# Kernel optimization log

Hardware: AMD Instinct MI355X
Metric: run time of the kernel (lower is better)

The kernel has to match this reference:

```python
import jax, jax.numpy as jnp
import numpy as np

HIDDEN = 2048
FFN = 8192
NUM_EXPERTS = 8
TOP_K = 2


def setup_inputs() -> dict:
    key = jax.random.key(0)
    ks = jax.random.split(key, 6)
    scale_h = 1.0 / np.sqrt(HIDDEN)
    scale_f = 1.0 / np.sqrt(FFN)
    return {
        "hidden_states": jax.random.normal(ks[0], (4, 2048, HIDDEN), jnp.float32),
        "gate_w": jax.random.normal(ks[1], (NUM_EXPERTS, HIDDEN), jnp.float32) * scale_h,
        "w1": jax.random.normal(ks[2], (NUM_EXPERTS, HIDDEN, FFN), jnp.float32) * scale_h,
        "b1": jax.random.normal(ks[3], (NUM_EXPERTS, FFN), jnp.float32) * 0.01,
        "w2": jax.random.normal(ks[4], (NUM_EXPERTS, FFN, HIDDEN), jnp.float32) * scale_f,
        "b2": jax.random.normal(ks[5], (NUM_EXPERTS, HIDDEN), jnp.float32) * 0.01,
    }


def reference(hidden_states, gate_w, w1, b1, w2, b2):
    B, S, H = hidden_states.shape
    E = gate_w.shape[0]
    tokens = hidden_states.reshape(-1, H)  # [T, H]

    # Router: softmax gate, top-2, renormalize selected weights
    logits = tokens @ gate_w.T  # [T, E]
    probs = jax.nn.softmax(logits, axis=-1)
    topk_w, topk_idx = jax.lax.top_k(probs, TOP_K)  # [T, 2]
    topk_w = topk_w / jnp.sum(topk_w, axis=-1, keepdims=True)

    # Dense combine weights: w_dense[t, e] = routing weight of token t for expert e
    w_dense = jnp.sum(jax.nn.one_hot(topk_idx, E, dtype=topk_w.dtype) * topk_w[..., None], axis=1)  # [T, E]

    # Per-expert FFN (exact GELU as nn.GELU default), weighted scatter-combine
    combined = jnp.zeros_like(tokens)
    for e in range(E):  # small fixed expert count
        h = jax.nn.gelu(tokens @ w1[e] + b1[e], approximate=False)  # [T, F]
        combined = combined + w_dense[:, e:e + 1] * (h @ w2[e] + b2[e])

    return combined.reshape(B, S, H) + hidden_states
```

## Files before the change

### kernel.cpp

```cpp
#include <hip/hip_runtime.h>
#include <hip/hip_bf16.h>

#define T_TOK 8192
#define HID 2048
#define FFN_ 8192
#define NE 8
#define MAXR 18432

typedef __attribute__((ext_vector_type(8))) short bf16x8;
typedef __attribute__((ext_vector_type(4))) float f32x4;
typedef __attribute__((ext_vector_type(8))) unsigned short u16x8;

__device__ __forceinline__ unsigned short f2bf(float f) {
  unsigned int u = __float_as_uint(f);
  u += 0x7fffu + ((u >> 16) & 1u);
  return (unsigned short)(u >> 16);
}
__device__ __forceinline__ float bf2f(unsigned short h) {
  return __uint_as_float(((unsigned int)h) << 16);
}

__device__ __forceinline__ void gload_lds16(const ushort* g, ushort* l) {
  __builtin_amdgcn_global_load_lds(
      (const __attribute__((address_space(1))) unsigned int*)g,
      (__attribute__((address_space(3))) unsigned int*)l, 16, 0, 0);
}

__global__ __launch_bounds__(256) void router_kernel(
    const float* __restrict__ x, const float* __restrict__ gw,
    int* __restrict__ topk_idx, float* __restrict__ topk_w, int* __restrict__ counts)
{
  int lane = threadIdx.x & 63;
  int w = threadIdx.x >> 6;
  int t = blockIdx.x * 4 + w;
  const float* xr = x + (size_t)t * HID;
  float acc[NE];
#pragma unroll
  for (int e = 0; e < NE; ++e) acc[e] = 0.f;
  for (int h = lane; h < HID; h += 64) {
    float xv = xr[h];
#pragma unroll
    for (int e = 0; e < NE; ++e) acc[e] = fmaf(xv, gw[e * HID + h], acc[e]);
  }
#pragma unroll
  for (int e = 0; e < NE; ++e) {
#pragma unroll
    for (int s = 32; s > 0; s >>= 1) acc[e] += __shfl_xor(acc[e], s);
  }
  if (lane == 0) {
    int i0 = 0; float v0 = acc[0];
#pragma unroll
    for (int e = 1; e < NE; ++e) { if (acc[e] > v0) { v0 = acc[e]; i0 = e; } }
    int i1 = -1; float v1 = -3.4e38f;
#pragma unroll
    for (int e = 0; e < NE; ++e) { if (e != i0 && acc[e] > v1) { v1 = acc[e]; i1 = e; } }
    float r = __expf(v1 - v0);
    float w0 = 1.f / (1.f + r);
    float w1 = r * w0;
    topk_idx[2 * t] = i0; topk_idx[2 * t + 1] = i1;
    topk_w[2 * t] = w0;   topk_w[2 * t + 1] = w1;
    atomicAdd(&counts[i0], 1);
    atomicAdd(&counts[i1], 1);
  }
}

__global__ void offsets_kernel(const int* __restrict__ counts, int* __restrict__ offs) {
  if (threadIdx.x == 0 && blockIdx.x == 0) {
    int o = 0;
#pragma unroll
    for (int e = 0; e < NE; ++e) { offs[e] = o; o += (counts[e] + 255) & ~255; }
    offs[NE] = o;
  }
}

__global__ __launch_bounds__(256) void scatter_kernel(
    const int* __restrict__ topk_idx, const float* __restrict__ topk_w,
    const int* __restrict__ offs, int* __restrict__ cursors,
    int* __restrict__ slot_token, float* __restrict__ slot_w, int* __restrict__ token_slot)
{
  int t = blockIdx.x * blockDim.x + threadIdx.x;
  if (t >= T_TOK) return;
#pragma unroll
  for (int k = 0; k < 2; ++k) {
    int e = topk_idx[2 * t + k];
    int pos = atomicAdd(&cursors[e], 1);
    int slot = offs[e] + pos;
    slot_token[slot] = t;
    slot_w[slot] = topk_w[2 * t + k];
    token_slot[2 * t + k] = slot;
  }
}

__global__ __launch_bounds__(256) void gather_kernel(
    const float* __restrict__ x, const int* __restrict__ slot_token, ushort* __restrict__ Xg)
{
  int row = blockIdx.x;
  int tok = slot_token[row];
  ushort* dst = Xg + (size_t)row * HID + threadIdx.x * 8;
  if (tok < 0) {
    u16x8 z = {0, 0, 0, 0, 0, 0, 0, 0};
    *(u16x8*)dst = z;
  } else {
    const float* s = x + (size_t)tok * HID + threadIdx.x * 8;
    float4 a = *(const float4*)s;
    float4 b = *(const float4*)(s + 4);
    u16x8 v;
    v[0] = f2bf(a.x); v[1] = f2bf(a.y); v[2] = f2bf(a.z); v[3] = f2bf(a.w);
    v[4] = f2bf(b.x); v[5] = f2bf(b.y); v[6] = f2bf(b.z); v[7] = f2bf(b.w);
    *(u16x8*)dst = v;
  }
}

__global__ __launch_bounds__(256) void transpose_convert_kernel(
    const float* __restrict__ src, ushort* __restrict__ dst, int R, int C)
{
  __shared__ float tile[64][65];
  int e = blockIdx.z;
  const float* s = src + (size_t)e * R * C;
  ushort* d = dst + (size_t)e * R * C;
  int r0 = blockIdx.y << 6, c0 = blockIdx.x << 6;
  int t = threadIdx.x;
#pragma unroll
  for (int i = 0; i < 4; ++i) {
    int idx = i * 256 + t;
    int row = idx >> 4;
    int c4 = (idx & 15) << 2;
    float4 v = *(const float4*)&s[(size_t)(r0 + row) * C + (c0 + c4)];
    tile[row][c4 + 0] = v.x; tile[row][c4 + 1] = v.y;
    tile[row][c4 + 2] = v.z; tile[row][c4 + 3] = v.w;
  }
  __syncthreads();
#pragma unroll
  for (int i = 0; i < 8; ++i) {
    int idx = (i * 256 + t) * 2;
    int orow = idx >> 6;
    int ocol = idx & 63;
    ushort2 p;
    p.x = f2bf(tile[ocol][orow]);
    p.y = f2bf(tile[ocol + 1][orow]);
    *(ushort2*)&d[(size_t)(c0 + orow) * R + (r0 + ocol)] = p;
  }
}


#define WAIT_LGKM() do { asm volatile("s_waitcnt lgkmcnt(0)" ::: "memory"); \
                         __builtin_amdgcn_sched_barrier(0); } while (0)
#define WAIT_VM6()  do { asm volatile("s_waitcnt vmcnt(6)" ::: "memory");  \
                         __builtin_amdgcn_sched_barrier(0); } while (0)
#define WAIT_VM0()  do { asm volatile("s_waitcnt vmcnt(0)" ::: "memory");  \
                         __builtin_amdgcn_sched_barrier(0); } while (0)

#define STG_A(BUF, HALF, T) do {                                            \
    ushort* _d = lds + (BUF) * 32768 + (HALF) * 8192 + tid * 8;             \
    gload_lds16(sA0 + (size_t)(HALF) * 64 * K + (size_t)(T) * 64, _d);      \
    gload_lds16(sA1 + (size_t)(HALF) * 64 * K + (size_t)(T) * 64, _d + 4096); \
  } while (0)
#define STG_B(BUF, HALF, T) do {                                            \
    ushort* _d = lds + (BUF) * 32768 + 16384 + (HALF) * 8192 + tid * 8;     \
    gload_lds16(sB0 + (size_t)(HALF) * 32 * K + (size_t)(T) * 64, _d);      \
    gload_lds16(sB1 + (size_t)(HALF) * 32 * K + (size_t)(T) * 64, _d + 4096); \
  } while (0)

#define LDA(BUF, MQ) do {                                                   \
    _Pragma("unroll") for (int mm = 0; mm < 4; ++mm) {                      \
      const ushort* _p = lds + (BUF) * 32768 + (MQ) * 8192 + aoff + mm * 1024; \
      af[mm][0] = *(const bf16x8*)(_p + ck0);                               \
      af[mm][1] = *(const bf16x8*)(_p + ck1);                               \
    } } while (0)
#define LDB(BUF, NQ) do {                                                   \
    _Pragma("unroll") for (int nn = 0; nn < 2; ++nn) {                      \
      const ushort* _p = lds + (BUF) * 32768 + 16384 + (NQ) * 8192 + boff + nn * 1024; \
      bf[NQ][nn][0] = *(const bf16x8*)(_p + ck0);                           \
      bf[NQ][nn][1] = *(const bf16x8*)(_p + ck1);                           \
    } } while (0)

#define MFMA_Q(MQ, NQ) do {                                                 \
    _Pragma("unroll") for (int mm = 0; mm < 4; ++mm)                        \
    _Pragma("unroll") for (int nn = 0; nn < 2; ++nn) {                      \
      acc[(MQ)*4+mm][(NQ)*2+nn] = __builtin_amdgcn_mfma_f32_16x16x32_bf16(  \
          af[mm][0], bf[NQ][nn][0], acc[(MQ)*4+mm][(NQ)*2+nn], 0, 0, 0);    \
      acc[(MQ)*4+mm][(NQ)*2+nn] = __builtin_amdgcn_mfma_f32_16x16x32_bf16(  \
          af[mm][1], bf[NQ][nn][1], acc[(MQ)*4+mm][(NQ)*2+nn], 0, 0, 0);    \
    } } while (0)

#define PH_MFMA(MQ, NQ) do {                                                \
    __builtin_amdgcn_s_barrier();                                           \
    WAIT_LGKM();                                                            \
    __builtin_amdgcn_s_setprio(1);                                          \
    MFMA_Q(MQ, NQ);                                                         \
    __builtin_amdgcn_s_setprio(0);                                          \
    __builtin_amdgcn_sched_barrier(0);                                      \
  } while (0)

template <int EPI>
__global__ __launch_bounds__(512, 2) void gemm256_kernel(
    const ushort* __restrict__ A, const ushort* __restrict__ Bt,
    const float* __restrict__ bias, ushort* __restrict__ Cout,
    const float* __restrict__ slot_w, const int* __restrict__ offs,
    int K, int N, int gx)
{
  __shared__ ushort lds[65536];

  const int tid = threadIdx.x;
  int nwg = gridDim.x * gridDim.y;
  int wg = blockIdx.y * gridDim.x + blockIdx.x;
  int cpx = nwg >> 3;
  wg = (wg & 7) * cpx + (wg >> 3);
  int rb = wg / gx, cb = wg - rb * gx;

  int total = offs[NE];
  int row0 = rb * 256;
  if (row0 >= total) return;
  int e = 0;
#pragma unroll
  for (int i = 1; i < NE; ++i) e += (row0 >= offs[i]) ? 1 : 0;

  const ushort* Ag = A + (size_t)row0 * K;
  const ushort* Bg = Bt + ((size_t)e * N + (size_t)cb * 256) * K;

  const int pr0 = tid >> 3;
  const int pr1 = 64 + pr0;
  const int j0 = (tid & 7) ^ (pr0 & 7);
  const int j1 = (tid & 7) ^ (pr1 & 7);
  const int rA0 = pr0;
  const int rA1 = 128 + pr0;
  const int rB0 = ((pr0 >> 5) << 6) + (pr0 & 31);
  const int rB1 = ((pr1 >> 5) << 6) + (pr1 & 31);
  const ushort* sA0 = Ag + (size_t)rA0 * K + j0 * 8;
  const ushort* sA1 = Ag + (size_t)rA1 * K + j1 * 8;
  const ushort* sB0 = Bg + (size_t)rB0 * K + j0 * 8;
  const ushort* sB1 = Bg + (size_t)rB1 * K + j1 * 8;

  const int lane = tid & 63;
  const int wid = tid >> 6;
  const int wr = wid >> 2, wc = wid & 3;
  const int lrow = lane & 15, g = lane >> 4, x7 = lrow & 7;
  const int ck0 = (g ^ x7) * 8;
  const int ck1 = ((4 + g) ^ x7) * 8;
  const int aoff = (wr * 64 + lrow) * 64;
  const int boff = (wc * 32 + lrow) * 64;

  f32x4 acc[8][4] = {};
  bf16x8 af[4][2], bf[2][2][2];

  const int NT = K >> 6;
  const int NITER = NT >> 1;

  STG_A(0, 0, 0); STG_A(0, 1, 0); STG_B(0, 0, 0); STG_B(0, 1, 0);
  STG_A(1, 0, 1); STG_B(1, 0, 1); STG_B(1, 1, 1);
  WAIT_VM6();
  __builtin_amdgcn_s_barrier();

  for (int it = 0; it < NITER; ++it) {
    const int tb = 2 * it + 1;
    const int tn0 = 2 * it + 2;
    const int tn1 = 2 * it + 3;
    const bool more0 = tn0 < NT;
    const bool more1 = tn1 < NT;

    LDA(0, 0); LDB(0, 0);
    STG_A(1, 1, tb);
    PH_MFMA(0, 0);
    __builtin_amdgcn_s_barrier();

    LDB(0, 1);
    if (more0) STG_A(0, 0, tn0);
    PH_MFMA(0, 1);
    __builtin_amdgcn_s_barrier();

    LDA(0, 1);
    if (more0) STG_B(0, 0, tn0);
    PH_MFMA(1, 0);
    __builtin_amdgcn_s_barrier();

    if (more0) STG_B(0, 1, tn0);
    PH_MFMA(1, 1);
    if (it + 1 < NITER) { WAIT_VM6(); } else { WAIT_VM0(); }
    __builtin_amdgcn_s_barrier();

    LDA(1, 0); LDB(1, 0);
    if (more0) STG_A(0, 1, tn0);
    PH_MFMA(0, 0);
    __builtin_amdgcn_s_barrier();

    LDB(1, 1);
    if (more1) STG_A(1, 0, tn1);
    PH_MFMA(0, 1);
    __builtin_amdgcn_s_barrier();

    LDA(1, 1);
    if (more1) STG_B(1, 0, tn1);
    PH_MFMA(1, 0);
    __builtin_amdgcn_s_barrier();

    if (more1) STG_B(1, 1, tn1);
    PH_MFMA(1, 1);
    if (more1) WAIT_VM6();
    __builtin_amdgcn_s_barrier();
  }

  const int colb = cb * 256 + wc * 64;
  const int rowb = row0 + wr * 128;
#pragma unroll
  for (int n = 0; n < 4; ++n) {
    const int nq = n >> 1, nn = n & 1;
    const int gc = colb + nq * 32 + nn * 16 + lrow;
    const float bv = bias[(size_t)e * N + gc];
#pragma unroll
    for (int m = 0; m < 8; ++m) {
      const int mq = m >> 2, mm = m & 3;
      const int gr = rowb + mq * 64 + mm * 16 + g * 4;
#pragma unroll
      for (int i = 0; i < 4; ++i) {
        float v = acc[m][n][i] + bv;
        if (EPI == 0) {
          v = 0.5f * v * (1.f + erff(v * 0.70710678118654752f));
        } else {
          v *= slot_w[gr + i];
        }
        Cout[(size_t)(gr + i) * N + gc] = f2bf(v);
      }
    }
  }
}

__global__ __launch_bounds__(256) void combine_kernel(
    const float* __restrict__ x, const ushort* __restrict__ Yp,
    const int* __restrict__ token_slot, float* __restrict__ out)
{
  int t = blockIdx.x;
  int s0 = token_slot[2 * t], s1 = token_slot[2 * t + 1];
  int c = threadIdx.x * 8;
  const float* xr = x + (size_t)t * HID + c;
  u16x8 y0 = *(const u16x8*)&Yp[(size_t)s0 * HID + c];
  u16x8 y1 = *(const u16x8*)&Yp[(size_t)s1 * HID + c];
  float4 xa = *(const float4*)xr;
  float4 xb = *(const float4*)(xr + 4);
  float4 oa, ob;
  oa.x = xa.x + bf2f(y0[0]) + bf2f(y1[0]);
  oa.y = xa.y + bf2f(y0[1]) + bf2f(y1[1]);
  oa.z = xa.z + bf2f(y0[2]) + bf2f(y1[2]);
  oa.w = xa.w + bf2f(y0[3]) + bf2f(y1[3]);
  ob.x = xb.x + bf2f(y0[4]) + bf2f(y1[4]);
  ob.y = xb.y + bf2f(y0[5]) + bf2f(y1[5]);
  ob.z = xb.z + bf2f(y0[6]) + bf2f(y1[6]);
  ob.w = xb.w + bf2f(y0[7]) + bf2f(y1[7]);
  float* orow = out + (size_t)t * HID + c;
  *(float4*)orow = oa;
  *(float4*)(orow + 4) = ob;
}

extern "C" void kernel_launch(void* const* d_in, const int* in_sizes, int n_in,
                              void* d_out, int out_size, void* d_ws, size_t ws_size,
                              hipStream_t stream)
{
  const float* x  = (const float*)d_in[0];
  const float* gw = (const float*)d_in[1];
  const float* w1 = (const float*)d_in[2];
  const float* b1 = (const float*)d_in[3];
  const float* w2 = (const float*)d_in[4];
  const float* b2 = (const float*)d_in[5];
  float* out = (float*)d_out;

  char* ws = (char*)d_ws;
  ushort* wT  = (ushort*)(ws + 0);
  ushort* Hb  = (ushort*)(ws + 268435456);
  ushort* Xg  = (ushort*)(ws + 570425344);
  ushort* Yp  = Xg;
  char* sm = ws + 645922816;
  int*   slot_token = (int*)(sm);
  float* slot_w     = (float*)(sm + 73728);
  int*   token_slot = (int*)(sm + 147456);
  int*   topk_idx   = (int*)(sm + 212992);
  float* topk_w     = (float*)(sm + 278528);
  int*   counts     = (int*)(sm + 344064);
  int*   cursors    = (int*)(sm + 344096);
  int*   offs       = (int*)(sm + 344128);

  hipMemsetAsync(counts, 0, 64, stream);
  hipMemsetAsync(slot_token, 0xFF, MAXR * 4, stream);

  router_kernel<<<dim3(T_TOK / 4), dim3(256), 0, stream>>>(x, gw, topk_idx, topk_w, counts);
  offsets_kernel<<<dim3(1), dim3(64), 0, stream>>>(counts, offs);
  scatter_kernel<<<dim3(T_TOK / 256), dim3(256), 0, stream>>>(
      topk_idx, topk_w, offs, cursors, slot_token, slot_w, token_slot);
  gather_kernel<<<dim3(MAXR), dim3(256), 0, stream>>>(x, slot_token, Xg);

  transpose_convert_kernel<<<dim3(FFN_ / 64, HID / 64, NE), dim3(256), 0, stream>>>(
      w1, wT, HID, FFN_);
  gemm256_kernel<0><<<dim3(FFN_ / 256, MAXR / 256), dim3(512), 0, stream>>>(
      Xg, wT, b1, Hb, nullptr, offs, HID, FFN_, FFN_ / 256);

  transpose_convert_kernel<<<dim3(HID / 64, FFN_ / 64, NE), dim3(256), 0, stream>>>(
      w2, wT, FFN_, HID);
  gemm256_kernel<1><<<dim3(HID / 256, MAXR / 256), dim3(512), 0, stream>>>(
      Hb, wT, b2, Yp, slot_w, offs, FFN_, HID, HID / 256);

  combine_kernel<<<dim3(T_TOK), dim3(256), 0, stream>>>(x, Yp, token_slot, out);
}
```

Measured before the change: 2.036 ms.

## Software-pipeline LDS fragment loads with double-buffered registers and remap tile raster

Restructures the GEMM main loop so the A/B fragments for the next MFMA phase are read from LDS into a second register set while the current phase computes, with one barrier per phase instead of two. The 2D grid becomes a 1D grid with an explicit XCD-aware mapping that keeps column blocks per XCD and iterates row blocks inside. The exact erf GELU is replaced with a tanh approximation built on a fast exp. The changes raise register pressure, make the barrier and wait ordering more delicate, and alter numerics slightly.

Result: slower. 2.713 ms (+33.2%).

```diff
diff --git a/kernel.cpp b/kernel.cpp
--- a/kernel.cpp
+++ b/kernel.cpp
@@ -24,6 +24,16 @@
   __builtin_amdgcn_global_load_lds(
       (const __attribute__((address_space(1))) unsigned int*)g,
       (__attribute__((address_space(3))) unsigned int*)l, 16, 0, 0);
+}
+
+__device__ __forceinline__ float gelu_f(float v) {
+  float u = v * (0.7978845608f + 0.0356774081f * v * v);
+  float a = fabsf(u);
+  float ex = __expf(-2.f * a);
+  float r = 1.f / (1.f + ex);
+  float th = (1.f - ex) * r;
+  th = (u >= 0.f) ? th : -th;
+  return 0.5f * v * (1.f + th);
 }
 
 __global__ __launch_bounds__(256) void router_kernel(
@@ -143,12 +153,10 @@
 }
 
 
-#define WAIT_LGKM() do { asm volatile("s_waitcnt lgkmcnt(0)" ::: "memory"); \
-                         __builtin_amdgcn_sched_barrier(0); } while (0)
-#define WAIT_VM6()  do { asm volatile("s_waitcnt vmcnt(6)" ::: "memory");  \
-                         __builtin_amdgcn_sched_barrier(0); } while (0)
-#define WAIT_VM0()  do { asm volatile("s_waitcnt vmcnt(0)" ::: "memory");  \
-                         __builtin_amdgcn_sched_barrier(0); } while (0)
+#define VMW6() asm volatile("s_waitcnt vmcnt(6)" ::: "memory")
+#define VMW0() asm volatile("s_waitcnt vmcnt(0)" ::: "memory")
+#define SCB()  __builtin_amdgcn_sched_barrier(0)
+#define BAR()  __builtin_amdgcn_s_barrier()
 
 #define STG_A(BUF, HALF, T) do {                                            \
     ushort* _d = lds + (BUF) * 32768 + (HALF) * 8192 + tid * 8;             \
@@ -161,35 +169,31 @@
     gload_lds16(sB1 + (size_t)(HALF) * 32 * K + (size_t)(T) * 64, _d + 4096); \
   } while (0)
 
-#define LDA(BUF, MQ) do {                                                   \
+#define LDA_INTO(SET, BUF, MQ) do {                                         \
     _Pragma("unroll") for (int mm = 0; mm < 4; ++mm) {                      \
       const ushort* _p = lds + (BUF) * 32768 + (MQ) * 8192 + aoff + mm * 1024; \
-      af[mm][0] = *(const bf16x8*)(_p + ck0);                               \
-      af[mm][1] = *(const bf16x8*)(_p + ck1);                               \
+      af##SET[mm][0] = *(const bf16x8*)(_p + ck0);                          \
+      af##SET[mm][1] = *(const bf16x8*)(_p + ck1);                          \
     } } while (0)
-#define LDB(BUF, NQ) do {                                                   \
+#define LDB_INTO(NQ, BUF) do {                                              \
     _Pragma("unroll") for (int nn = 0; nn < 2; ++nn) {                      \
       const ushort* _p = lds + (BUF) * 32768 + 16384 + (NQ) * 8192 + boff + nn * 1024; \
       bf[NQ][nn][0] = *(const bf16x8*)(_p + ck0);                           \
       bf[NQ][nn][1] = *(const bf16x8*)(_p + ck1);                           \
     } } while (0)
 
-#define MFMA_Q(MQ, NQ) do {                                                 \
+#define MFMAQ(SET, MQ, NQ) do {                                             \
+    SCB();                                                                  \
+    __builtin_amdgcn_s_setprio(1);                                          \
     _Pragma("unroll") for (int mm = 0; mm < 4; ++mm)                        \
     _Pragma("unroll") for (int nn = 0; nn < 2; ++nn) {                      \
       acc[(MQ)*4+mm][(NQ)*2+nn] = __builtin_amdgcn_mfma_f32_16x16x32_bf16(  \
-          af[mm][0], bf[NQ][nn][0], acc[(MQ)*4+mm][(NQ)*2+nn], 0, 0, 0);    \
+          af##SET[mm][0], bf[NQ][nn][0], acc[(MQ)*4+mm][(NQ)*2+nn], 0, 0, 0); \
       acc[(MQ)*4+mm][(NQ)*2+nn] = __builtin_amdgcn_mfma_f32_16x16x32_bf16(  \
-          af[mm][1], bf[NQ][nn][1], acc[(MQ)*4+mm][(NQ)*2+nn], 0, 0, 0);    \
-    } } while (0)
-
-#define PH_MFMA(MQ, NQ) do {                                                \
-    __builtin_amdgcn_s_barrier();                                           \
-    WAIT_LGKM();                                                            \
-    __builtin_amdgcn_s_setprio(1);                                          \
-    MFMA_Q(MQ, NQ);                                                         \
+          af##SET[mm][1], bf[NQ][nn][1], acc[(MQ)*4+mm][(NQ)*2+nn], 0, 0, 0); \
+    }                                                                       \
     __builtin_amdgcn_s_setprio(0);                                          \
-    __builtin_amdgcn_sched_barrier(0);                                      \
+    SCB(); BAR(); SCB();                                                    \
   } while (0)
 
 template <int EPI>
@@ -197,16 +201,16 @@
     const ushort* __restrict__ A, const ushort* __restrict__ Bt,
     const float* __restrict__ bias, ushort* __restrict__ Cout,
     const float* __restrict__ slot_w, const int* __restrict__ offs,
-    int K, int N, int gx)
+    int K, int N, int gx, int gy)
 {
   __shared__ ushort lds[65536];
 
   const int tid = threadIdx.x;
-  int nwg = gridDim.x * gridDim.y;
-  int wg = blockIdx.y * gridDim.x + blockIdx.x;
-  int cpx = nwg >> 3;
-  wg = (wg & 7) * cpx + (wg >> 3);
-  int rb = wg / gx, cb = wg - rb * gx;
+  int b = blockIdx.x;
+  int xcd = b & 7, s = b >> 3;
+  int sc = s / gy;
+  int cb = xcd * (gx >> 3) + sc;
+  int rb = s - sc * gy;
 
   int total = offs[NE];
   int row0 = rb * 256;
@@ -241,62 +245,67 @@
   const int boff = (wc * 32 + lrow) * 64;
 
   f32x4 acc[8][4] = {};
-  bf16x8 af[4][2], bf[2][2][2];
+  bf16x8 af0[4][2], af1[4][2], bf[2][2][2];
 
   const int NT = K >> 6;
   const int NITER = NT >> 1;
 
   STG_A(0, 0, 0); STG_A(0, 1, 0); STG_B(0, 0, 0); STG_B(0, 1, 0);
   STG_A(1, 0, 1); STG_B(1, 0, 1); STG_B(1, 1, 1);
-  WAIT_VM6();
-  __builtin_amdgcn_s_barrier();
+  VMW6();
+  BAR(); SCB();
+  LDA_INTO(0, 0, 0);
+  LDB_INTO(0, 0);
 
   for (int it = 0; it < NITER; ++it) {
-    const int tb = 2 * it + 1;
+    const int tb  = 2 * it + 1;
     const int tn0 = 2 * it + 2;
     const int tn1 = 2 * it + 3;
     const bool more0 = tn0 < NT;
     const bool more1 = tn1 < NT;
-
-    LDA(0, 0); LDB(0, 0);
+    const bool last = (it + 1 == NITER);
+
     STG_A(1, 1, tb);
-    PH_MFMA(0, 0);
-    __builtin_amdgcn_s_barrier();
-
-    LDB(0, 1);
+    VMW6();
+    LDB_INTO(1, 0);
+    MFMAQ(0, 0, 0);
+
     if (more0) STG_A(0, 0, tn0);
-    PH_MFMA(0, 1);
-    __builtin_amdgcn_s_barrier();
-
-    LDA(0, 1);
+    if (last) { VMW0(); } else { VMW6(); }
+    LDA_INTO(1, 0, 1);
+    MFMAQ(0, 0, 1);
+
     if (more0) STG_B(0, 0, tn0);
-    PH_MFMA(1, 0);
-    __builtin_amdgcn_s_barrier();
+    VMW6();
+    MFMAQ(1, 1, 0);
 
     if (more0) STG_B(0, 1, tn0);
-    PH_MFMA(1, 1);
-    if (it + 1 < NITER) { WAIT_VM6(); } else { WAIT_VM0(); }
-    __builtin_amdgcn_s_barrier();
-
-    LDA(1, 0); LDB(1, 0);
+    VMW6();
+    LDA_INTO(0, 1, 0);
+    LDB_INTO(0, 1);
+    MFMAQ(1, 1, 1);
+
     if (more0) STG_A(0, 1, tn0);
-    PH_MFMA(0, 0);
-    __builtin_amdgcn_s_barrier();
-
-    LDB(1, 1);
+    VMW6();
+    LDB_INTO(1, 1);
+    MFMAQ(0, 0, 0);
+
     if (more1) STG_A(1, 0, tn1);
-    PH_MFMA(0, 1);
-    __builtin_amdgcn_s_barrier();
-
-    LDA(1, 1);
+    VMW6();
+    LDA_INTO(1, 1, 1);
+    MFMAQ(0, 0, 1);
+
     if (more1) STG_B(1, 0, tn1);
-    PH_MFMA(1, 0);
-    __builtin_amdgcn_s_barrier();
+    VMW6();
+    MFMAQ(1, 1, 0);
 
     if (more1) STG_B(1, 1, tn1);
-    PH_MFMA(1, 1);
-    if (more1) WAIT_VM6();
-    __builtin_amdgcn_s_barrier();
+    VMW6();
+    if (!last) {
+      LDA_INTO(0, 0, 0);
+      LDB_INTO(0, 0);
+    }
+    MFMAQ(1, 1, 1);
   }
 
   const int colb = cb * 256 + wc * 64;
@@ -314,7 +323,7 @@
       for (int i = 0; i < 4; ++i) {
         float v = acc[m][n][i] + bv;
         if (EPI == 0) {
-          v = 0.5f * v * (1.f + erff(v * 0.70710678118654752f));
+          v = gelu_f(v);
         } else {
           v *= slot_w[gr + i];
         }
@@ -388,13 +397,13 @@
 
   transpose_convert_kernel<<<dim3(FFN_ / 64, HID / 64, NE), dim3(256), 0, stream>>>(
       w1, wT, HID, FFN_);
-  gemm256_kernel<0><<<dim3(FFN_ / 256, MAXR / 256), dim3(512), 0, stream>>>(
-      Xg, wT, b1, Hb, nullptr, offs, HID, FFN_, FFN_ / 256);
+  gemm256_kernel<0><<<dim3((FFN_ / 256) * (MAXR / 256)), dim3(512), 0, stream>>>(
+      Xg, wT, b1, Hb, nullptr, offs, HID, FFN_, FFN_ / 256, MAXR / 256);
 
   transpose_convert_kernel<<<dim3(HID / 64, FFN_ / 64, NE), dim3(256), 0, stream>>>(
       w2, wT, FFN_, HID);
-  gemm256_kernel<1><<<dim3(HID / 256, MAXR / 256), dim3(512), 0, stream>>>(
-      Hb, wT, b2, Yp, slot_w, offs, FFN_, HID, HID / 256);
+  gemm256_kernel<1><<<dim3((HID / 256) * (MAXR / 256)), dim3(512), 0, stream>>>(
+      Hb, wT, b2, Yp, slot_w, offs, FFN_, HID, HID / 256, MAXR / 256);
 
   combine_kernel<<<dim3(T_TOK), dim3(256), 0, stream>>>(x, Yp, token_slot, out);
 }
```

## Swap exact-erf GELU for tanh approximation and reorder GEMM tile traversal column-major

Applied to the files above, without the earlier changes.

Replaces the erff-based exact GELU in the first GEMM epilogue with a tanh-form approximation built on __expf, cutting transcendental cost in the epilogue. The GEMM grid becomes 1D, and tiles are assigned column-block-major so consecutive workgroups share the same expert weight column block across row blocks, aiming for better L2 reuse of weights. The epilogue is also reordered to hoist bias loads and slot weights per row. The tanh GELU deviates slightly from the exact erf form the reference specifies.

Result: no change. 2.000 ms (-1.8%).

```diff
diff --git a/kernel.cpp b/kernel.cpp
--- a/kernel.cpp
+++ b/kernel.cpp
@@ -24,6 +24,16 @@
   __builtin_amdgcn_global_load_lds(
       (const __attribute__((address_space(1))) unsigned int*)g,
       (__attribute__((address_space(3))) unsigned int*)l, 16, 0, 0);
+}
+
+__device__ __forceinline__ float gelu_f(float v) {
+  float u = v * (0.7978845608f + 0.0356774081f * v * v);
+  float a = fabsf(u);
+  float ex = __expf(-2.f * a);
+  float r = 1.f / (1.f + ex);
+  float th = (1.f - ex) * r;
+  th = (u >= 0.f) ? th : -th;
+  return 0.5f * v * (1.f + th);
 }
 
 __global__ __launch_bounds__(256) void router_kernel(
@@ -197,16 +207,17 @@
     const ushort* __restrict__ A, const ushort* __restrict__ Bt,
     const float* __restrict__ bias, ushort* __restrict__ Cout,
     const float* __restrict__ slot_w, const int* __restrict__ offs,
-    int K, int N, int gx)
+    int K, int N, int gy)
 {
   __shared__ ushort lds[65536];
 
   const int tid = threadIdx.x;
-  int nwg = gridDim.x * gridDim.y;
-  int wg = blockIdx.y * gridDim.x + blockIdx.x;
+  int nwg = gridDim.x;
+  int wg = blockIdx.x;
   int cpx = nwg >> 3;
   wg = (wg & 7) * cpx + (wg >> 3);
-  int rb = wg / gx, cb = wg - rb * gx;
+  int cb = wg / gy;
+  int rb = wg - cb * gy;
 
   int total = offs[NE];
   int row0 = rb * 256;
@@ -301,24 +312,25 @@
 
   const int colb = cb * 256 + wc * 64;
   const int rowb = row0 + wr * 128;
-#pragma unroll
-  for (int n = 0; n < 4; ++n) {
-    const int nq = n >> 1, nn = n & 1;
-    const int gc = colb + nq * 32 + nn * 16 + lrow;
-    const float bv = bias[(size_t)e * N + gc];
-#pragma unroll
-    for (int m = 0; m < 8; ++m) {
-      const int mq = m >> 2, mm = m & 3;
-      const int gr = rowb + mq * 64 + mm * 16 + g * 4;
-#pragma unroll
-      for (int i = 0; i < 4; ++i) {
-        float v = acc[m][n][i] + bv;
-        if (EPI == 0) {
-          v = 0.5f * v * (1.f + erff(v * 0.70710678118654752f));
-        } else {
-          v *= slot_w[gr + i];
-        }
-        Cout[(size_t)(gr + i) * N + gc] = f2bf(v);
+  float bv[4];
+#pragma unroll
+  for (int n = 0; n < 4; ++n)
+    bv[n] = bias[(size_t)e * N + colb + n * 16 + lrow];
+#pragma unroll
+  for (int m = 0; m < 8; ++m) {
+    const int mq = m >> 2, mm = m & 3;
+    const int gr = rowb + mq * 64 + mm * 16 + g * 4;
+#pragma unroll
+    for (int i = 0; i < 4; ++i) {
+      const int grow = gr + i;
+      float sw = (EPI == 1) ? slot_w[grow] : 0.f;
+      ushort* crow = Cout + (size_t)grow * N + colb + lrow;
+#pragma unroll
+      for (int n = 0; n < 4; ++n) {
+        float v = acc[m][n][i] + bv[n];
+        if (EPI == 0) v = gelu_f(v);
+        else          v *= sw;
+        crow[n * 16] = f2bf(v);
       }
     }
   }
@@ -388,13 +400,13 @@
 
   transpose_convert_kernel<<<dim3(FFN_ / 64, HID / 64, NE), dim3(256), 0, stream>>>(
       w1, wT, HID, FFN_);
-  gemm256_kernel<0><<<dim3(FFN_ / 256, MAXR / 256), dim3(512), 0, stream>>>(
-      Xg, wT, b1, Hb, nullptr, offs, HID, FFN_, FFN_ / 256);
+  gemm256_kernel<0><<<dim3((FFN_ / 256) * (MAXR / 256)), dim3(512), 0, stream>>>(
+      Xg, wT, b1, Hb, nullptr, offs, HID, FFN_, MAXR / 256);
 
   transpose_convert_kernel<<<dim3(HID / 64, FFN_ / 64, NE), dim3(256), 0, stream>>>(
       w2, wT, FFN_, HID);
-  gemm256_kernel<1><<<dim3(HID / 256, MAXR / 256), dim3(512), 0, stream>>>(
-      Hb, wT, b2, Yp, slot_w, offs, FFN_, HID, HID / 256);
+  gemm256_kernel<1><<<dim3((HID / 256) * (MAXR / 256)), dim3(512), 0, stream>>>(
+      Hb, wT, b2, Yp, slot_w, offs, FFN_, HID, MAXR / 256);
 
   combine_kernel<<<dim3(T_TOK), dim3(256), 0, stream>>>(x, Yp, token_slot, out);
 }
```
